# Optimization experiments

Measured on AMD Instinct MI355X. Metric: run time of the kernel, lower is better.

Reference implementation:

```python
import jax, jax.numpy as jnp
import numpy as np
import math

B, SQ, SK, H, NH = 8, 512, 512, 768, 12
DH = H // NH

def setup_inputs() -> dict:
    key = jax.random.key(0)
    ks = jax.random.split(key, 8)
    s = 1.0 / math.sqrt(H)
    return {
        "hidden_states": jax.random.normal(ks[0], (B, SQ, H), jnp.float32),
        "context": jax.random.normal(ks[1], (B, SK, H), jnp.float32),
        "attention_mask": jax.random.randint(ks[2], (B, SK), 0, 2, jnp.int32),
        "Wq": jax.random.normal(ks[3], (H, H), jnp.float32) * s,
        "bq": jnp.zeros((H,), jnp.float32),
        "Wk": jax.random.normal(ks[4], (H, H), jnp.float32) * s,
        "bk": jnp.zeros((H,), jnp.float32),
        "Wv": jax.random.normal(ks[5], (H, H), jnp.float32) * s,
        "bv": jnp.zeros((H,), jnp.float32),
        "abs_pos_emb": jax.random.normal(ks[6], (512, DH), jnp.float32),
    }

def _heads(x):
    # [B, S, H] -> [B, NH, S, DH]
    b, s, _ = x.shape
    return x.reshape(b, s, NH, DH).transpose(0, 2, 1, 3)

def reference(hidden_states, context, attention_mask, Wq, bq, Wk, bk, Wv, bv, abs_pos_emb):
    q = _heads(hidden_states @ Wq.T + bq)   # [B,NH,SQ,DH]
    k = _heads(context @ Wk.T + bk)         # [B,NH,SK,DH]
    v = _heads(context @ Wv.T + bv)         # [B,NH,SK,DH]
    scores = jnp.einsum('bhqd,bhkd->bhqk', q, k)
    pos_k = abs_pos_emb[:context.shape[1]]          # [SK, DH]
    pos_q = abs_pos_emb[:hidden_states.shape[1]]    # [SQ, DH]
    pos_scores = jnp.einsum('bhqd,kd->bhqk', q + pos_q[None, None], pos_k)
    scores = (scores + pos_scores) / jnp.sqrt(jnp.float32(DH))
    mask_bias = jnp.where(attention_mask[:, None, None, :] == 0,
                          -jnp.inf, 0.0).astype(scores.dtype)
    scores = scores + mask_bias
    probs = jax.nn.softmax(scores, axis=-1)  # dropout is identity in eval
    out = jnp.einsum('bhqk,bhkd->bhqd', probs, v)
    b, _, sq, _ = out.shape
    return out.transpose(0, 2, 1, 3).reshape(b, sq, NH * DH)
```

## Files before the change

### kernel.cpp

```cpp
#include <hip/hip_runtime.h>
#include <stdint.h>

#define B_   8
#define SQ_  512
#define SK_  512
#define H_   768
#define NH_  12
#define DH_  64
#define BH_  (B_*NH_)
#define M_   (B_*SQ_)
#define NTOT (3*H_)

typedef __attribute__((ext_vector_type(8))) short short8;
typedef __attribute__((ext_vector_type(4))) float floatx4;
typedef __attribute__((ext_vector_type(4))) unsigned int uint4v;
typedef __attribute__((ext_vector_type(4))) unsigned short ushort4v;

#define MFMA16(a, b, c) __builtin_amdgcn_mfma_f32_16x16x32_bf16((a), (b), (c), 0, 0, 0)

__device__ __forceinline__ unsigned short f2b(float f) {
  union { float f; unsigned u; } c; c.f = f;
  unsigned r = (c.u + 0x7fffu + ((c.u >> 16) & 1u)) >> 16;
  return (unsigned short)r;
}
__device__ __forceinline__ float b2f(unsigned short u) {
  union { float f; unsigned u; } c; c.u = ((unsigned)u) << 16;
  return c.f;
}
__device__ __forceinline__ short8 ld8(const unsigned short* p) {
  union { uint4v u; short8 s; } c;
  c.u = *(const uint4v*)p;
  return c.s;
}

#define SEG_X   (M_*H_)
#define SEG_XC  (2*SEG_X)
#define SEG_W1  (H_*H_)
#define SEG_WE  (SEG_XC + 3*SEG_W1)
#define SEG_BE  (SEG_WE + NTOT)
#define SEG_PE  (SEG_BE + SQ_*DH_)

__global__ __launch_bounds__(256) void pack_kernel(
    const float* __restrict__ hid, const float* __restrict__ ctx,
    const float* __restrict__ Wq, const float* __restrict__ Wk, const float* __restrict__ Wv,
    const float* __restrict__ bq, const float* __restrict__ bk, const float* __restrict__ bv,
    const float* __restrict__ pos,
    unsigned short* __restrict__ Xh, unsigned short* __restrict__ Xc,
    unsigned short* __restrict__ Wa, float* __restrict__ Ba,
    unsigned short* __restrict__ Pb)
{
  int i = (blockIdx.x * 256 + threadIdx.x) * 4;
  if (i < SEG_X) {
    floatx4 v = *(const floatx4*)(hid + i);
    ushort4v o = { f2b(v.x), f2b(v.y), f2b(v.z), f2b(v.w) };
    *(ushort4v*)(Xh + i) = o;
  } else if (i < SEG_XC) {
    int j = i - SEG_X;
    floatx4 v = *(const floatx4*)(ctx + j);
    ushort4v o = { f2b(v.x), f2b(v.y), f2b(v.z), f2b(v.w) };
    *(ushort4v*)(Xc + j) = o;
  } else if (i < SEG_WE) {
    int j = i - SEG_XC;
    const float* src; int o;
    if (j < SEG_W1)        { src = Wq; o = j; }
    else if (j < 2*SEG_W1) { src = Wk; o = j - SEG_W1; }
    else                   { src = Wv; o = j - 2*SEG_W1; }
    floatx4 v = *(const floatx4*)(src + o);
    ushort4v ov = { f2b(v.x), f2b(v.y), f2b(v.z), f2b(v.w) };
    *(ushort4v*)(Wa + j) = ov;
  } else if (i < SEG_BE) {
    int j = i - SEG_WE;
    #pragma unroll
    for (int t = 0; t < 4; ++t) {
      int jj = j + t;
      float v = (jj < H_) ? bq[jj] : (jj < 2*H_) ? bk[jj - H_] : bv[jj - 2*H_];
      Ba[jj] = v;
    }
  } else if (i < SEG_PE) {
    int j = i - SEG_BE;
    floatx4 v = *(const floatx4*)(pos + j);
    ushort4v o = { f2b(v.x), f2b(v.y), f2b(v.z), f2b(v.w) };
    *(ushort4v*)(Pb + j) = o;
  }
}

__global__ __launch_bounds__(256) void qkv_gemm(
    const unsigned short* __restrict__ Xh, const unsigned short* __restrict__ Xc,
    const unsigned short* __restrict__ W,  const float* __restrict__ bias,
    const unsigned short* __restrict__ Pb,
    unsigned short* __restrict__ qw, unsigned short* __restrict__ kw,
    unsigned short* __restrict__ vt)
{
  __shared__ unsigned short As[128][72];
  __shared__ unsigned short Bs[128][72];

  int bx = blockIdx.x;
  int xcd = bx & 7, j = bx >> 3;
  int bm = (xcd >> 1) * 8 + j / 9;
  int bn = (xcd & 1) * 9 + j % 9;
  const unsigned short* X = (bn < 6) ? Xh : Xc;
  bool isV = (bn >= 12);
  int m0 = bm * 128, n0 = bn * 128;

  int tid = threadIdx.x;
  int lane = tid & 63, wave = tid >> 6;
  int wm = (wave & 1) * 64, wn = (wave >> 1) * 64;
  int lc16 = lane & 15, quad = lane >> 4, kk = quad * 8;
  int srow = tid >> 3, sch = (tid & 7) * 8;

  unsigned short (*TA)[72] = isV ? As : Bs;
  unsigned short (*TB)[72] = isV ? Bs : As;
  int oa = isV ? wm : wn;
  int ob = isV ? wn : wm;

  floatx4 acc[4][4];
  #pragma unroll
  for (int i = 0; i < 4; ++i)
    #pragma unroll
    for (int jj = 0; jj < 4; ++jj) acc[i][jj] = (floatx4){0.f, 0.f, 0.f, 0.f};

  uint4v a[4], b[4];
  #pragma unroll
  for (int rp = 0; rp < 4; ++rp) {
    a[rp] = *(const uint4v*)&X[(m0 + srow + rp * 32) * H_ + sch];
    b[rp] = *(const uint4v*)&W[(n0 + srow + rp * 32) * H_ + sch];
  }

  for (int k0 = 0; k0 < H_; k0 += 64) {
    __syncthreads();
    #pragma unroll
    for (int rp = 0; rp < 4; ++rp) {
      *(uint4v*)&As[srow + rp * 32][sch] = a[rp];
      *(uint4v*)&Bs[srow + rp * 32][sch] = b[rp];
    }
    __syncthreads();

    if (k0 + 64 < H_) {
      #pragma unroll
      for (int rp = 0; rp < 4; ++rp) {
        a[rp] = *(const uint4v*)&X[(m0 + srow + rp * 32) * H_ + k0 + 64 + sch];
        b[rp] = *(const uint4v*)&W[(n0 + srow + rp * 32) * H_ + k0 + 64 + sch];
      }
    }

    #pragma unroll
    for (int s = 0; s < 2; ++s) {
      short8 af[4], bf[4];
      #pragma unroll
      for (int i = 0; i < 4; ++i) af[i] = ld8(&TA[oa + i * 16 + lc16][s * 32 + kk]);
      #pragma unroll
      for (int i = 0; i < 4; ++i) bf[i] = ld8(&TB[ob + i * 16 + lc16][s * 32 + kk]);
      #pragma unroll
      for (int mi = 0; mi < 4; ++mi)
        #pragma unroll
        for (int ni = 0; ni < 4; ++ni)
          acc[mi][ni] = MFMA16(af[mi], bf[ni], acc[mi][ni]);
    }
  }

  if (!isV) {
    #pragma unroll
    for (int mi = 0; mi < 4; ++mi) {
      #pragma unroll
      for (int ni = 0; ni < 4; ++ni) {
        int gn0 = n0 + wn + mi * 16 + quad * 4;
        int gs  = m0 + wm + ni * 16 + lc16;
        int bidx = gs >> 9, s0 = gs & 511;
        floatx4 bv4 = *(const floatx4*)&bias[gn0];
        ushort4v o;
        if (gn0 < H_) {
          int h = gn0 >> 6, d0 = gn0 & 63;
          #pragma unroll
          for (int r = 0; r < 4; ++r) o[r] = f2b(acc[mi][ni][r] + bv4[r]);
          *(ushort4v*)(qw + (((bidx * NH_ + h) << 9) + s0) * DH_ + d0) = o;
        } else {
          int g = gn0 - H_;
          int h = g >> 6, d0 = g & 63;
          ushort4v pk = *(const ushort4v*)(Pb + s0 * DH_ + d0);
          #pragma unroll
          for (int r = 0; r < 4; ++r) o[r] = f2b(acc[mi][ni][r] + bv4[r] + b2f(pk[r]));
          *(ushort4v*)(kw + (((bidx * NH_ + h) << 9) + s0) * DH_ + d0) = o;
        }
      }
    }
  } else {
    #pragma unroll
    for (int mi = 0; mi < 4; ++mi) {
      #pragma unroll
      for (int ni = 0; ni < 4; ++ni) {
        int gm0 = m0 + wm + mi * 16 + quad * 4;
        int gn  = n0 + wn + ni * 16 + lc16;
        float bv = bias[gn];
        int bidx = gm0 >> 9, s0 = gm0 & 511;
        int g = gn - 2 * H_;
        int h = g >> 6, d = g & 63;
        ushort4v pk;
        #pragma unroll
        for (int r = 0; r < 4; ++r) pk[r] = f2b(acc[mi][ni][r] + bv);
        *(ushort4v*)(vt + ((bidx * NH_ + h) * DH_ + d) * SK_ + s0) = pk;
      }
    }
  }
}

#define SCALE2 0.18033688011112042f
#define CPAD 136

__global__ __launch_bounds__(256) void attn_kernel(
    const unsigned short* __restrict__ qw, const unsigned short* __restrict__ kw,
    const unsigned short* __restrict__ vt, const unsigned short* __restrict__ posb,
    const int* __restrict__ mask, float* __restrict__ out)
{
  __shared__ unsigned short Sc[2][64][CPAD];
  __shared__ float mb2[SK_];
  __shared__ float red[64][4];

  int bx = blockIdx.x;
  int bh = bx % 96, qt = bx / 96;
  int b = bh / NH_, h = bh - b * NH_;
  int tid = threadIdx.x, lane = tid & 63, wave = tid >> 6;
  int lc16 = lane & 15, quad = lane >> 4, kk = quad * 8;

  for (int i = tid; i < SK_; i += 256)
    mb2[i] = mask[(b << 9) + i] ? 0.0f : -100000.0f;

  const unsigned short* qbase = qw + ((bh << 9) + qt * 64) * DH_;
  const unsigned short* pqb   = posb + (qt * 64) * DH_;
  short8 aq[4][2], ap[4][2];
  #pragma unroll
  for (int rt = 0; rt < 4; ++rt) {
    const unsigned short* qr = qbase + (rt * 16 + lc16) * DH_;
    const unsigned short* pr = pqb + (rt * 16 + lc16) * DH_;
    aq[rt][0] = ld8(qr + kk);
    aq[rt][1] = ld8(qr + 32 + kk);
    ap[rt][0] = ld8(pr + kk);
    ap[rt][1] = ld8(pr + 32 + kk);
  }

  const unsigned short* kwb = kw + ((bh << 9)) * DH_;
  const unsigned short* vb0 = vt + (bh * DH_ + wave * 16 + lc16) * SK_;
  float rs[4] = {0.f, 0.f, 0.f, 0.f};
  floatx4 o[4];
  #pragma unroll
  for (int i = 0; i < 4; ++i) o[i] = (floatx4){0.f, 0.f, 0.f, 0.f};

  short8 cb0, cb1, cp0, cp1, nb0, nb1, np0, np1;
  {
    int kcol = wave * 32;
    const unsigned short* kb = kwb + kcol * DH_;
    const unsigned short* pb = posb + kcol * DH_;
    cb0 = ld8(kb + lc16 * DH_ + kk);
    cb1 = ld8(kb + lc16 * DH_ + 32 + kk);
    cp0 = ld8(pb + lc16 * DH_ + kk);
    cp1 = ld8(pb + lc16 * DH_ + 32 + kk);
  }

  __syncthreads();

  for (int chunk = 0; chunk < 4; ++chunk) {
    unsigned short (*S)[CPAD] = Sc[chunk & 1];

    short8 vf[4];
    #pragma unroll
    for (int ks = 0; ks < 4; ++ks) vf[ks] = ld8(vb0 + chunk * 128 + ks * 32 + kk);

    #pragma unroll
    for (int ct = 0; ct < 2; ++ct) {
      int s = chunk * 2 + ct;
      if (s < 7) {
        int kcol = ((s + 1) >> 1) * 128 + wave * 32 + ((s + 1) & 1) * 16;
        const unsigned short* kb = kwb + kcol * DH_;
        const unsigned short* pb = posb + kcol * DH_;
        nb0 = ld8(kb + lc16 * DH_ + kk);
        nb1 = ld8(kb + lc16 * DH_ + 32 + kk);
        np0 = ld8(pb + lc16 * DH_ + kk);
        np1 = ld8(pb + lc16 * DH_ + 32 + kk);
      }
      int kcol = chunk * 128 + wave * 32 + ct * 16;
      floatx4 mk = *(const floatx4*)&mb2[kcol + quad * 4];
      floatx4 c[4];
      #pragma unroll
      for (int rt = 0; rt < 4; ++rt) {
        c[rt] = (floatx4){0.f, 0.f, 0.f, 0.f};
        c[rt] = MFMA16(cb0, aq[rt][0], c[rt]);
        c[rt] = MFMA16(cb1, aq[rt][1], c[rt]);
        c[rt] = MFMA16(cp0, ap[rt][0], c[rt]);
        c[rt] = MFMA16(cp1, ap[rt][1], c[rt]);
      }
      int lcol = wave * 32 + ct * 16 + quad * 4;
      #pragma unroll
      for (int rt = 0; rt < 4; ++rt) {
        ushort4v pv;
        float sum = 0.f;
        #pragma unroll
        for (int r = 0; r < 4; ++r) {
          float e = __builtin_exp2f(c[rt][r] * SCALE2 + mk[r]);
          sum += e;
          pv[r] = f2b(e);
        }
        rs[rt] += sum;
        *(ushort4v*)&S[rt * 16 + lc16][lcol] = pv;
      }
      cb0 = nb0; cb1 = nb1; cp0 = np0; cp1 = np1;
    }
    __syncthreads();

    #pragma unroll
    for (int ks = 0; ks < 4; ++ks) {
      #pragma unroll
      for (int rt = 0; rt < 4; ++rt) {
        short8 pa = ld8(&S[rt * 16 + lc16][ks * 32 + kk]);
        o[rt] = MFMA16(pa, vf[ks], o[rt]);
      }
    }
  }

  #pragma unroll
  for (int rt = 0; rt < 4; ++rt) {
    rs[rt] += __shfl_xor(rs[rt], 16, 64);
    rs[rt] += __shfl_xor(rs[rt], 32, 64);
  }
  if (quad == 0) {
    #pragma unroll
    for (int rt = 0; rt < 4; ++rt) red[rt * 16 + lc16][wave] = rs[rt];
  }
  __syncthreads();

  #pragma unroll
  for (int rt = 0; rt < 4; ++rt) {
    #pragma unroll
    for (int r = 0; r < 4; ++r) {
      int sl = rt * 16 + quad * 4 + r;
      float inv = 1.0f / (red[sl][0] + red[sl][1] + red[sl][2] + red[sl][3]);
      int s = qt * 64 + sl;
      out[((b << 9) + s) * H_ + h * DH_ + wave * 16 + lc16] = o[rt][r] * inv;
    }
  }
}

extern "C" void kernel_launch(void* const* d_in, const int* in_sizes, int n_in,
                              void* d_out, int out_size, void* d_ws, size_t ws_size,
                              hipStream_t stream) {
  (void)in_sizes; (void)n_in; (void)out_size; (void)ws_size;
  const float* hid  = (const float*)d_in[0];
  const float* ctx  = (const float*)d_in[1];
  const int*   mask = (const int*)d_in[2];
  const float* Wq   = (const float*)d_in[3];
  const float* bq   = (const float*)d_in[4];
  const float* Wk   = (const float*)d_in[5];
  const float* bk   = (const float*)d_in[6];
  const float* Wv   = (const float*)d_in[7];
  const float* bv   = (const float*)d_in[8];
  const float* pos  = (const float*)d_in[9];

  char* ws = (char*)d_ws;
  size_t off = 0;
  auto alloc = [&](size_t bytes) { char* p = ws + off; off = (off + bytes + 255) & ~(size_t)255; return p; };
  unsigned short* Xh = (unsigned short*)alloc((size_t)SEG_X * 2);
  unsigned short* Xc = (unsigned short*)alloc((size_t)SEG_X * 2);
  unsigned short* Wa = (unsigned short*)alloc((size_t)3 * SEG_W1 * 2);
  float*          Ba = (float*)alloc((size_t)NTOT * 4);
  unsigned short* qw = (unsigned short*)alloc((size_t)BH_ * SQ_ * DH_ * 2);
  unsigned short* kw = (unsigned short*)alloc((size_t)BH_ * SK_ * DH_ * 2);
  unsigned short* vt = (unsigned short*)alloc((size_t)BH_ * DH_ * SK_ * 2);
  unsigned short* Pb = (unsigned short*)alloc((size_t)SQ_ * DH_ * 2);

  int pack_blocks = (SEG_PE / 4 + 255) / 256;
  pack_kernel<<<pack_blocks, 256, 0, stream>>>(hid, ctx, Wq, Wk, Wv, bq, bk, bv, pos, Xh, Xc, Wa, Ba, Pb);
  qkv_gemm<<<32 * 18, 256, 0, stream>>>(Xh, Xc, Wa, Ba, Pb, qw, kw, vt);
  attn_kernel<<<BH_ * 8, 256, 0, stream>>>(qw, kw, vt, Pb, mask, (float*)d_out);
}
```

Measured before the change: 154.9 us.

## Use direct global-to-LDS loads in QKV GEMM and raise MFMA wave priority

The QKV projection GEMM now stages tiles with global_load_lds straight into shared memory instead of loading into registers and storing to LDS. This removes the register staging and the padded LDS rows. It also drops the software prefetch of the next tile, so each k-step waits for its own loads, and the unpadded 64-wide rows may cause LDS bank conflicts on the fragment reads. Separately, the attention kernel wraps its MFMA blocks in s_setprio so those waves get issue priority over the others.

```diff
diff --git a/kernel.cpp b/kernel.cpp
--- a/kernel.cpp
+++ b/kernel.cpp
@@ -31,6 +31,11 @@
   union { uint4v u; short8 s; } c;
   c.u = *(const uint4v*)p;
   return c.s;
+}
+__device__ __forceinline__ void gl_lds16(const unsigned short* g, unsigned short* l) {
+  __builtin_amdgcn_global_load_lds(
+      (const __attribute__((address_space(1))) unsigned int*)g,
+      (__attribute__((address_space(3))) unsigned int*)l, 16, 0, 0);
 }
 
 #define SEG_X   (M_*H_)
@@ -91,8 +96,8 @@
     unsigned short* __restrict__ qw, unsigned short* __restrict__ kw,
     unsigned short* __restrict__ vt)
 {
-  __shared__ unsigned short As[128][72];
-  __shared__ unsigned short Bs[128][72];
+  __shared__ unsigned short As[128][64];
+  __shared__ unsigned short Bs[128][64];
 
   int bx = blockIdx.x;
   int xcd = bx & 7, j = bx >> 3;
@@ -106,10 +111,11 @@
   int lane = tid & 63, wave = tid >> 6;
   int wm = (wave & 1) * 64, wn = (wave >> 1) * 64;
   int lc16 = lane & 15, quad = lane >> 4, kk = quad * 8;
-  int srow = tid >> 3, sch = (tid & 7) * 8;
-
-  unsigned short (*TA)[72] = isV ? As : Bs;
-  unsigned short (*TB)[72] = isV ? Bs : As;
+  int srow8 = lane >> 3;
+  int scol  = (lane & 7) * 8;
+
+  unsigned short (*TA)[64] = isV ? As : Bs;
+  unsigned short (*TB)[64] = isV ? Bs : As;
   int oa = isV ? wm : wn;
   int ob = isV ? wn : wm;
 
@@ -119,29 +125,16 @@
     #pragma unroll
     for (int jj = 0; jj < 4; ++jj) acc[i][jj] = (floatx4){0.f, 0.f, 0.f, 0.f};
 
-  uint4v a[4], b[4];
-  #pragma unroll
-  for (int rp = 0; rp < 4; ++rp) {
-    a[rp] = *(const uint4v*)&X[(m0 + srow + rp * 32) * H_ + sch];
-    b[rp] = *(const uint4v*)&W[(n0 + srow + rp * 32) * H_ + sch];
-  }
+  int rbase = wave * 32;
 
   for (int k0 = 0; k0 < H_; k0 += 64) {
+    #pragma unroll
+    for (int c = 0; c < 4; ++c) {
+      int r = rbase + c * 8;
+      gl_lds16(&X[(m0 + r + srow8) * H_ + k0 + scol], &As[r][0]);
+      gl_lds16(&W[(n0 + r + srow8) * H_ + k0 + scol], &Bs[r][0]);
+    }
     __syncthreads();
-    #pragma unroll
-    for (int rp = 0; rp < 4; ++rp) {
-      *(uint4v*)&As[srow + rp * 32][sch] = a[rp];
-      *(uint4v*)&Bs[srow + rp * 32][sch] = b[rp];
-    }
-    __syncthreads();
-
-    if (k0 + 64 < H_) {
-      #pragma unroll
-      for (int rp = 0; rp < 4; ++rp) {
-        a[rp] = *(const uint4v*)&X[(m0 + srow + rp * 32) * H_ + k0 + 64 + sch];
-        b[rp] = *(const uint4v*)&W[(n0 + srow + rp * 32) * H_ + k0 + 64 + sch];
-      }
-    }
 
     #pragma unroll
     for (int s = 0; s < 2; ++s) {
@@ -156,6 +149,7 @@
         for (int ni = 0; ni < 4; ++ni)
           acc[mi][ni] = MFMA16(af[mi], bf[ni], acc[mi][ni]);
     }
+    __syncthreads();
   }
 
   if (!isV) {
@@ -279,6 +273,7 @@
       int kcol = chunk * 128 + wave * 32 + ct * 16;
       floatx4 mk = *(const floatx4*)&mb2[kcol + quad * 4];
       floatx4 c[4];
+      __builtin_amdgcn_s_setprio(1);
       #pragma unroll
       for (int rt = 0; rt < 4; ++rt) {
         c[rt] = (floatx4){0.f, 0.f, 0.f, 0.f};
@@ -287,6 +282,7 @@
         c[rt] = MFMA16(cp0, ap[rt][0], c[rt]);
         c[rt] = MFMA16(cp1, ap[rt][1], c[rt]);
       }
+      __builtin_amdgcn_s_setprio(0);
       int lcol = wave * 32 + ct * 16 + quad * 4;
       #pragma unroll
       for (int rt = 0; rt < 4; ++rt) {
@@ -305,6 +301,7 @@
     }
     __syncthreads();
 
+    __builtin_amdgcn_s_setprio(1);
     #pragma unroll
     for (int ks = 0; ks < 4; ++ks) {
       #pragma unroll
@@ -313,6 +310,7 @@
         o[rt] = MFMA16(pa, vf[ks], o[rt]);
       }
     }
+    __builtin_amdgcn_s_setprio(0);
   }
 
   #pragma unroll
```

Measured after the change: 166.2 us. 7.2% more time.

## Fuse fp32-to-bf16 packing into QKV GEMM loads and raise MFMA wave priority

Applied to the files above, without the earlier changes.

Removes the separate pack kernel. The QKV GEMM now reads fp32 activations and weights directly and converts them to bf16 in registers before staging them in LDS. Bias and positional embeddings are read in fp32 in the epilogue, and the first 16 GEMM blocks also write the bf16 positional table that the attention kernel needs. This saves one launch and the full round trip through the bf16 staging buffers, at the cost of twice the global bytes per GEMM tile load. The attention kernel also wraps its MFMA sections in s_setprio to favour matrix issue across waves.

```diff
diff --git a/kernel.cpp b/kernel.cpp
--- a/kernel.cpp
+++ b/kernel.cpp
@@ -32,75 +32,48 @@
   c.u = *(const uint4v*)p;
   return c.s;
 }
-
-#define SEG_X   (M_*H_)
-#define SEG_XC  (2*SEG_X)
-#define SEG_W1  (H_*H_)
-#define SEG_WE  (SEG_XC + 3*SEG_W1)
-#define SEG_BE  (SEG_WE + NTOT)
-#define SEG_PE  (SEG_BE + SQ_*DH_)
-
-__global__ __launch_bounds__(256) void pack_kernel(
+__device__ __forceinline__ uint4v cvt8(floatx4 lo, floatx4 hi) {
+  uint4v r;
+  r.x = (unsigned)f2b(lo.x) | ((unsigned)f2b(lo.y) << 16);
+  r.y = (unsigned)f2b(lo.z) | ((unsigned)f2b(lo.w) << 16);
+  r.z = (unsigned)f2b(hi.x) | ((unsigned)f2b(hi.y) << 16);
+  r.w = (unsigned)f2b(hi.z) | ((unsigned)f2b(hi.w) << 16);
+  return r;
+}
+
+__global__ __launch_bounds__(256) void qkv_gemm(
     const float* __restrict__ hid, const float* __restrict__ ctx,
     const float* __restrict__ Wq, const float* __restrict__ Wk, const float* __restrict__ Wv,
     const float* __restrict__ bq, const float* __restrict__ bk, const float* __restrict__ bv,
     const float* __restrict__ pos,
-    unsigned short* __restrict__ Xh, unsigned short* __restrict__ Xc,
-    unsigned short* __restrict__ Wa, float* __restrict__ Ba,
-    unsigned short* __restrict__ Pb)
-{
-  int i = (blockIdx.x * 256 + threadIdx.x) * 4;
-  if (i < SEG_X) {
-    floatx4 v = *(const floatx4*)(hid + i);
-    ushort4v o = { f2b(v.x), f2b(v.y), f2b(v.z), f2b(v.w) };
-    *(ushort4v*)(Xh + i) = o;
-  } else if (i < SEG_XC) {
-    int j = i - SEG_X;
-    floatx4 v = *(const floatx4*)(ctx + j);
-    ushort4v o = { f2b(v.x), f2b(v.y), f2b(v.z), f2b(v.w) };
-    *(ushort4v*)(Xc + j) = o;
-  } else if (i < SEG_WE) {
-    int j = i - SEG_XC;
-    const float* src; int o;
-    if (j < SEG_W1)        { src = Wq; o = j; }
-    else if (j < 2*SEG_W1) { src = Wk; o = j - SEG_W1; }
-    else                   { src = Wv; o = j - 2*SEG_W1; }
-    floatx4 v = *(const floatx4*)(src + o);
-    ushort4v ov = { f2b(v.x), f2b(v.y), f2b(v.z), f2b(v.w) };
-    *(ushort4v*)(Wa + j) = ov;
-  } else if (i < SEG_BE) {
-    int j = i - SEG_WE;
-    #pragma unroll
-    for (int t = 0; t < 4; ++t) {
-      int jj = j + t;
-      float v = (jj < H_) ? bq[jj] : (jj < 2*H_) ? bk[jj - H_] : bv[jj - 2*H_];
-      Ba[jj] = v;
-    }
-  } else if (i < SEG_PE) {
-    int j = i - SEG_BE;
-    floatx4 v = *(const floatx4*)(pos + j);
-    ushort4v o = { f2b(v.x), f2b(v.y), f2b(v.z), f2b(v.w) };
-    *(ushort4v*)(Pb + j) = o;
-  }
-}
-
-__global__ __launch_bounds__(256) void qkv_gemm(
-    const unsigned short* __restrict__ Xh, const unsigned short* __restrict__ Xc,
-    const unsigned short* __restrict__ W,  const float* __restrict__ bias,
-    const unsigned short* __restrict__ Pb,
     unsigned short* __restrict__ qw, unsigned short* __restrict__ kw,
-    unsigned short* __restrict__ vt)
+    unsigned short* __restrict__ vt, unsigned short* __restrict__ Pb)
 {
   __shared__ unsigned short As[128][72];
   __shared__ unsigned short Bs[128][72];
 
   int bx = blockIdx.x;
+
+  if (bx < 16) {
+    int base = (bx * 256 + (int)threadIdx.x) * 8;
+    floatx4 p0 = *(const floatx4*)(pos + base);
+    floatx4 p1 = *(const floatx4*)(pos + base + 4);
+    ushort4v o0 = { f2b(p0.x), f2b(p0.y), f2b(p0.z), f2b(p0.w) };
+    ushort4v o1 = { f2b(p1.x), f2b(p1.y), f2b(p1.z), f2b(p1.w) };
+    *(ushort4v*)(Pb + base)     = o0;
+    *(ushort4v*)(Pb + base + 4) = o1;
+  }
+
   int xcd = bx & 7, j = bx >> 3;
   int bm = (xcd >> 1) * 8 + j / 9;
   int bn = (xcd & 1) * 9 + j % 9;
-  const unsigned short* X = (bn < 6) ? Xh : Xc;
-  bool isV = (bn >= 12);
-  int m0 = bm * 128, n0 = bn * 128;
+  const float* X = (bn < 6) ? hid : ctx;
+  int wsel = bn / 6;
+  const float* Wp = (wsel == 0) ? Wq : (wsel == 1) ? Wk : Wv;
+  const float* bp = (wsel == 0) ? bq : (wsel == 1) ? bk : bv;
+  int nloc0 = (bn - wsel * 6) * 128;
+  bool isV = (wsel == 2);
+  int m0 = bm * 128;
 
   int tid = threadIdx.x;
   int lane = tid & 63, wave = tid >> 6;
@@ -119,11 +92,18 @@
     #pragma unroll
     for (int jj = 0; jj < 4; ++jj) acc[i][jj] = (floatx4){0.f, 0.f, 0.f, 0.f};
 
+  const float* Xb = X  + (size_t)(m0    + srow) * H_ + sch;
+  const float* Wb = Wp + (size_t)(nloc0 + srow) * H_ + sch;
+
   uint4v a[4], b[4];
   #pragma unroll
   for (int rp = 0; rp < 4; ++rp) {
-    a[rp] = *(const uint4v*)&X[(m0 + srow + rp * 32) * H_ + sch];
-    b[rp] = *(const uint4v*)&W[(n0 + srow + rp * 32) * H_ + sch];
+    floatx4 x0 = *(const floatx4*)(Xb + rp * 32 * H_);
+    floatx4 x1 = *(const floatx4*)(Xb + rp * 32 * H_ + 4);
+    floatx4 w0 = *(const floatx4*)(Wb + rp * 32 * H_);
+    floatx4 w1 = *(const floatx4*)(Wb + rp * 32 * H_ + 4);
+    a[rp] = cvt8(x0, x1);
+    b[rp] = cvt8(w0, w1);
   }
 
   for (int k0 = 0; k0 < H_; k0 += 64) {
@@ -138,8 +118,12 @@
     if (k0 + 64 < H_) {
       #pragma unroll
       for (int rp = 0; rp < 4; ++rp) {
-        a[rp] = *(const uint4v*)&X[(m0 + srow + rp * 32) * H_ + k0 + 64 + sch];
-        b[rp] = *(const uint4v*)&W[(n0 + srow + rp * 32) * H_ + k0 + 64 + sch];
+        floatx4 x0 = *(const floatx4*)(Xb + rp * 32 * H_ + k0 + 64);
+        floatx4 x1 = *(const floatx4*)(Xb + rp * 32 * H_ + k0 + 68);
+        floatx4 w0 = *(const floatx4*)(Wb + rp * 32 * H_ + k0 + 64);
+        floatx4 w1 = *(const floatx4*)(Wb + rp * 32 * H_ + k0 + 68);
+        a[rp] = cvt8(x0, x1);
+        b[rp] = cvt8(w0, w1);
       }
     }
 
@@ -163,22 +147,20 @@
     for (int mi = 0; mi < 4; ++mi) {
       #pragma unroll
       for (int ni = 0; ni < 4; ++ni) {
-        int gn0 = n0 + wn + mi * 16 + quad * 4;
+        int gnl = nloc0 + wn + mi * 16 + quad * 4;
         int gs  = m0 + wm + ni * 16 + lc16;
         int bidx = gs >> 9, s0 = gs & 511;
-        floatx4 bv4 = *(const floatx4*)&bias[gn0];
+        floatx4 bv4 = *(const floatx4*)&bp[gnl];
+        int h = gnl >> 6, d0 = gnl & 63;
         ushort4v o;
-        if (gn0 < H_) {
-          int h = gn0 >> 6, d0 = gn0 & 63;
+        if (wsel == 0) {
           #pragma unroll
           for (int r = 0; r < 4; ++r) o[r] = f2b(acc[mi][ni][r] + bv4[r]);
           *(ushort4v*)(qw + (((bidx * NH_ + h) << 9) + s0) * DH_ + d0) = o;
         } else {
-          int g = gn0 - H_;
-          int h = g >> 6, d0 = g & 63;
-          ushort4v pk = *(const ushort4v*)(Pb + s0 * DH_ + d0);
+          floatx4 pk = *(const floatx4*)&pos[s0 * DH_ + d0];
           #pragma unroll
-          for (int r = 0; r < 4; ++r) o[r] = f2b(acc[mi][ni][r] + bv4[r] + b2f(pk[r]));
+          for (int r = 0; r < 4; ++r) o[r] = f2b(acc[mi][ni][r] + bv4[r] + pk[r]);
           *(ushort4v*)(kw + (((bidx * NH_ + h) << 9) + s0) * DH_ + d0) = o;
         }
       }
@@ -189,14 +171,13 @@
       #pragma unroll
       for (int ni = 0; ni < 4; ++ni) {
         int gm0 = m0 + wm + mi * 16 + quad * 4;
-        int gn  = n0 + wn + ni * 16 + lc16;
-        float bv = bias[gn];
+        int gnl = nloc0 + wn + ni * 16 + lc16;
+        float bvs = bp[gnl];
         int bidx = gm0 >> 9, s0 = gm0 & 511;
-        int g = gn - 2 * H_;
-        int h = g >> 6, d = g & 63;
+        int h = gnl >> 6, d = gnl & 63;
         ushort4v pk;
         #pragma unroll
-        for (int r = 0; r < 4; ++r) pk[r] = f2b(acc[mi][ni][r] + bv);
+        for (int r = 0; r < 4; ++r) pk[r] = f2b(acc[mi][ni][r] + bvs);
         *(ushort4v*)(vt + ((bidx * NH_ + h) * DH_ + d) * SK_ + s0) = pk;
       }
     }
@@ -279,6 +260,7 @@
       int kcol = chunk * 128 + wave * 32 + ct * 16;
       floatx4 mk = *(const floatx4*)&mb2[kcol + quad * 4];
       floatx4 c[4];
+      __builtin_amdgcn_s_setprio(1);
       #pragma unroll
       for (int rt = 0; rt < 4; ++rt) {
         c[rt] = (floatx4){0.f, 0.f, 0.f, 0.f};
@@ -287,6 +269,7 @@
         c[rt] = MFMA16(cp0, ap[rt][0], c[rt]);
         c[rt] = MFMA16(cp1, ap[rt][1], c[rt]);
       }
+      __builtin_amdgcn_s_setprio(0);
       int lcol = wave * 32 + ct * 16 + quad * 4;
       #pragma unroll
       for (int rt = 0; rt < 4; ++rt) {
@@ -305,6 +288,7 @@
     }
     __syncthreads();
 
+    __builtin_amdgcn_s_setprio(1);
     #pragma unroll
     for (int ks = 0; ks < 4; ++ks) {
       #pragma unroll
@@ -313,6 +297,7 @@
         o[rt] = MFMA16(pa, vf[ks], o[rt]);
       }
     }
+    __builtin_amdgcn_s_setprio(0);
   }
 
   #pragma unroll
@@ -356,17 +341,11 @@
   char* ws = (char*)d_ws;
   size_t off = 0;
   auto alloc = [&](size_t bytes) { char* p = ws + off; off = (off + bytes + 255) & ~(size_t)255; return p; };
-  unsigned short* Xh = (unsigned short*)alloc((size_t)SEG_X * 2);
-  unsigned short* Xc = (unsigned short*)alloc((size_t)SEG_X * 2);
-  unsigned short* Wa = (unsigned short*)alloc((size_t)3 * SEG_W1 * 2);
-  float*          Ba = (float*)alloc((size_t)NTOT * 4);
   unsigned short* qw = (unsigned short*)alloc((size_t)BH_ * SQ_ * DH_ * 2);
   unsigned short* kw = (unsigned short*)alloc((size_t)BH_ * SK_ * DH_ * 2);
   unsigned short* vt = (unsigned short*)alloc((size_t)BH_ * DH_ * SK_ * 2);
   unsigned short* Pb = (unsigned short*)alloc((size_t)SQ_ * DH_ * 2);
 
-  int pack_blocks = (SEG_PE / 4 + 255) / 256;
-  pack_kernel<<<pack_blocks, 256, 0, stream>>>(hid, ctx, Wq, Wk, Wv, bq, bk, bv, pos, Xh, Xc, Wa, Ba, Pb);
-  qkv_gemm<<<32 * 18, 256, 0, stream>>>(Xh, Xc, Wa, Ba, Pb, qw, kw, vt);
+  qkv_gemm<<<32 * 18, 256, 0, stream>>>(hid, ctx, Wq, Wk, Wv, bq, bk, bv, pos, qw, kw, vt, Pb);
   attn_kernel<<<BH_ * 8, 256, 0, stream>>>(qw, kw, vt, Pb, mask, (float*)d_out);
 }
```

Measured after the change: 155.1 us. No clear change (+0.1%).
